# Performance work log

Measured on AMD Instinct MI355X. Metric: run time of the kernel, lower is better.

## Reference

```python
import jax, jax.numpy as jnp
import numpy as np

BETA = 0.5

def gelu(x):
    return jax.nn.gelu(x, approximate=False)  # torch F.gelu default is exact erf

def setup_inputs() -> dict:
    key = jax.random.key(0)
    ks = jax.random.split(key, 10)
    N, F, PH, P, D, H, C, E = 50000, 128, 64, 8, 4, 128, 10, 1600000
    s = 0.05
    return {
        "x": jax.random.normal(ks[0], (N, F), jnp.float32),
        "W_proj": jax.random.normal(ks[1], (PH, F), jnp.float32) * s,
        "b_proj": jnp.zeros((PH,), jnp.float32),
        "W_x": jax.random.normal(ks[2], (H, F), jnp.float32) * s,
        "b_x": jnp.zeros((H,), jnp.float32),
        "W_path": jax.random.normal(ks[3], (H, D * PH), jnp.float32) * s,
        "b_path": jnp.zeros((H,), jnp.float32),
        "W_A": jax.random.normal(ks[4], (H, N), jnp.float32) * s,
        "b_A": jnp.zeros((H,), jnp.float32),
        "W_end": jax.random.normal(ks[5], (C, H), jnp.float32) * s,
        "b_end": jnp.zeros((C,), jnp.float32),
        "index": jax.random.randint(ks[6], (N, P, D), 0, N, jnp.int64)
                 if jax.config.jax_enable_x64 else jax.random.randint(ks[6], (N, P, D), 0, N, jnp.int32),
        "edge_index": jax.random.randint(ks[7], (2, E), 0, N, jnp.int32),
    }

def reference(x, W_proj, b_proj, W_x, b_x, W_path, b_path, W_A, b_A, W_end, b_end, index, edge_index):
    N = x.shape[0]
    # path projection then per-node path gather: [N, P, D, PH]
    pp = x @ W_proj.T + b_proj
    path = pp[index]
    Np, P, D, PH = path.shape
    # node MLP (dropout off in eval)
    h = gelu(x @ W_x.T + b_x)  # [N, H]
    # concat path encoder: [N, P, D*PH] -> [N, P, H]
    pi = gelu(path.reshape(Np, P, D * PH) @ W_path.T + b_path)
    # dot-product path attention with softmax over path dim
    att = jax.nn.softmax(jnp.einsum('nh,nph->np', h, pi), axis=-1)
    path_agg = jnp.einsum('np,nph->nh', att, pi)
    # sparse adjacency (COO, weights=1) times Linear weight: A @ W_A.T + b_A
    M = W_A.T  # [N, H]
    A_x = jax.ops.segment_sum(M[edge_index[1]], edge_index[0], num_segments=N) + b_A
    out = (1.0 - BETA) * (path_agg + h) + BETA * A_x
    out = gelu(out)
    return out @ W_end.T + b_end
```

## Files before the change

### kernel.cpp

```cpp
#include <hip/hip_runtime.h>
#include <hip/hip_bf16.h>
#include <math.h>

#define NF   128
#define NPH  64
#define NP   8
#define ND   4
#define NH   128
#define NC   10
#define BCAP 2560

typedef __bf16 bf16;
typedef __attribute__((ext_vector_type(4))) __bf16 bf16x4;
typedef __attribute__((ext_vector_type(8))) __bf16 bf16x8;
typedef __attribute__((ext_vector_type(4))) float f32x4;

template<int CTRL>
__device__ __forceinline__ float dpp_add(float x) {
    int t = __builtin_amdgcn_update_dpp(0, __float_as_int(x), CTRL, 0xf, 0xf, false);
    return x + __int_as_float(t);
}
__device__ __forceinline__ float row16_sum(float x) {
    x = dpp_add<0x121>(x);
    x = dpp_add<0x122>(x);
    x = dpp_add<0x124>(x);
    x = dpp_add<0x128>(x);
    return x;
}

__device__ __forceinline__ float gelu_fast(float x) {
    float z = fabsf(x) * 0.70710678118654752f;
    float t = __builtin_amdgcn_rcpf(1.0f + 0.47047f * z);
    float poly = t * (0.3480242f + t * (-0.0958798f + t * 0.7478556f));
    float erfv = 1.0f - poly * __expf(-z * z);
    float s = copysignf(erfv, x);
    return 0.5f * x * (1.0f + s);
}

#define GLOAD_LDS16(g, l)                                                     \
    __builtin_amdgcn_global_load_lds(                                         \
        (const __attribute__((address_space(1))) unsigned int*)(g),           \
        (__attribute__((address_space(3))) unsigned int*)(l), 16, 0, 0)

__device__ __forceinline__ bf16x8 cvt8(float4 a, float4 b) {
    bf16x8 r;
    r[0] = (bf16)a.x; r[1] = (bf16)a.y; r[2] = (bf16)a.z; r[3] = (bf16)a.w;
    r[4] = (bf16)b.x; r[5] = (bf16)b.y; r[6] = (bf16)b.z; r[7] = (bf16)b.w;
    return r;
}

__device__ __forceinline__ void add8(float* a, uint4 v) {
    a[0] += __uint_as_float(v.x << 16);  a[1] += __uint_as_float(v.x & 0xffff0000u);
    a[2] += __uint_as_float(v.y << 16);  a[3] += __uint_as_float(v.y & 0xffff0000u);
    a[4] += __uint_as_float(v.z << 16);  a[5] += __uint_as_float(v.z & 0xffff0000u);
    a[6] += __uint_as_float(v.w << 16);  a[7] += __uint_as_float(v.w & 0xffff0000u);
}

__global__ __launch_bounds__(256) void k_front(
    const float* __restrict__ x,
    const float* __restrict__ Wproj, const float* __restrict__ bproj,
    const float* __restrict__ Wx,    const float* __restrict__ bx,
    bf16* __restrict__ pp, float* __restrict__ h,
    const float* __restrict__ WA, bf16* __restrict__ Mb,
    const int* __restrict__ esrc, const int* __restrict__ edst,
    int* __restrict__ gcur, unsigned* __restrict__ pairs,
    int N, int E, int nbuck, int nbP, int nbT)
{
    __shared__ alignas(16) char smem[33280];
    const int tid = threadIdx.x;

    const int bid = blockIdx.x;
    const int two = 2 * nbP;
    int cls, idx;
    if (bid < two) { cls = bid & 1; idx = bid >> 1; }
    else           { cls = 1; idx = nbP + (bid - two); }

    if (cls == 0) {
        bf16* x_s = (bf16*)smem;
        const int w = tid >> 6, l = tid & 63;
        const int c = l & 15, g = l >> 4;

        bf16x8 bfr[3][4];
        float bias[3];
        #pragma unroll
        for (int t = 0; t < 3; ++t) {
            int ch = (w * 3 + t) * 16 + c;
            const float* wr = (ch < NPH) ? &Wproj[(size_t)ch * NF]
                                         : &Wx[(size_t)(ch - NPH) * NF];
            bias[t] = (ch < NPH) ? bproj[ch] : bx[ch - NPH];
            #pragma unroll
            for (int ks = 0; ks < 4; ++ks) {
                const float* src = wr + ks * 32 + g * 8;
                bfr[t][ks] = cvt8(*(const float4*)src, *(const float4*)(src + 4));
            }
        }

        const int n0 = idx * 64;
        #pragma unroll
        for (int rr = 0; rr < 8; ++rr) {
            int id  = rr * 256 + tid;
            int row = id >> 5, c4 = id & 31;
            float4 v = make_float4(0.f, 0.f, 0.f, 0.f);
            if (n0 + row < N) v = *(const float4*)&x[(size_t)(n0 + row) * NF + c4 * 4];
            bf16x4 o;
            o[0] = (bf16)v.x; o[1] = (bf16)v.y; o[2] = (bf16)v.z; o[3] = (bf16)v.w;
            *(bf16x4*)&x_s[row * 136 + c4 * 4] = o;
        }
        __syncthreads();

        f32x4 acc[4][3] = {};
        #pragma unroll
        for (int rt = 0; rt < 4; ++rt)
            #pragma unroll
            for (int ks = 0; ks < 4; ++ks) {
                bf16x8 a = *(const bf16x8*)&x_s[(rt * 16 + c) * 136 + ks * 32 + g * 8];
                #pragma unroll
                for (int t = 0; t < 3; ++t)
                    acc[rt][t] = __builtin_amdgcn_mfma_f32_16x16x32_bf16(
                        a, bfr[t][ks], acc[rt][t], 0, 0, 0);
            }

        #pragma unroll
        for (int rt = 0; rt < 4; ++rt) {
            #pragma unroll
            for (int t = 0; t < 3; ++t) {
                int ch = (w * 3 + t) * 16 + c;
                #pragma unroll
                for (int i = 0; i < 4; ++i) {
                    int n = n0 + rt * 16 + g * 4 + i;
                    if (n >= N) continue;
                    float v = acc[rt][t][i] + bias[t];
                    if (ch < NPH) pp[(size_t)n * NPH + ch] = (bf16)v;
                    else          h[(size_t)n * NH + (ch - NPH)] = gelu_fast(v);
                }
            }
        }
    } else if (idx < nbT) {
        float* tt = (float*)smem;
        const int n0 = idx * 64;
        const int w = tid >> 6, l = tid & 63;
        #pragma unroll
        for (int rep = 0; rep < 32; ++rep) {
            int hh = rep * 4 + w;
            int n  = n0 + l;
            tt[hh * 65 + l] = (n < N) ? WA[(size_t)hh * N + n] : 0.f;
        }
        __syncthreads();
        #pragma unroll
        for (int rep = 0; rep < 32; ++rep) {
            int n_l = rep * 2 + (tid >> 7);
            int n   = n0 + n_l;
            if (n < N) Mb[(size_t)n * NH + (tid & 127)] = (bf16)tt[(tid & 127) * 65 + n_l];
        }
    } else {
        int* cnt  = (int*)smem;
        int* bofs = cnt + 800;
        const int tile = (idx - nbT) * 4096;
        for (int i = tid; i < nbuck; i += 256) cnt[i] = 0;
        __syncthreads();
        #pragma unroll
        for (int k = 0; k < 16; ++k) {
            int i = tile + k * 256 + tid;
            if (i < E) atomicAdd(&cnt[esrc[i] >> 6], 1);
        }
        __syncthreads();
        for (int i = tid; i < nbuck; i += 256) {
            int c = cnt[i];
            bofs[i] = c ? atomicAdd(&gcur[i], c) : 0;
            cnt[i] = 0;
        }
        __syncthreads();
        #pragma unroll
        for (int k = 0; k < 16; ++k) {
            int i = tile + k * 256 + tid;
            if (i < E) {
                int s = esrc[i], b = s >> 6;
                int r = atomicAdd(&cnt[b], 1);
                pairs[(size_t)b * BCAP + bofs[b] + r] =
                    ((unsigned)(s & 63) << 16) | (unsigned)edst[i];
            }
        }
    }
}

__global__ __launch_bounds__(256, 3) void k_mid2(
    const unsigned* __restrict__ pairs, const int* __restrict__ gcur,
    const bf16* __restrict__ Mb, const float* __restrict__ bA,
    float* __restrict__ axbuf2,
    const bf16* __restrict__ pp, const float* __restrict__ h,
    const float* __restrict__ Wpath, const float* __restrict__ bpath,
    const int* __restrict__ index, float* __restrict__ aggbuf,
    int N, int E, int nbuck, int nrounds)
{
    __shared__ alignas(16) char smem[37376];
    const int tid = threadIdx.x;

    const int bid = blockIdx.x;
    const int two = 2 * nbuck;
    int cls, idx;
    if (bid < two) { cls = bid & 1; idx = bid >> 1; }
    else           { cls = 0; idx = nbuck + (bid - two); }

    if (cls == 1) {
        int* hist  = (int*)smem;
        int* sc    = hist + 64;
        int* cur   = hist + 128;
        unsigned short* dstl = (unsigned short*)(smem + 768);
        const int b = idx, t = tid;
        const int cnt = gcur[b];
        const unsigned* pb = pairs + (size_t)b * BCAP;

        if (t < 64) hist[t] = 0;
        __syncthreads();
        for (int j = t; j < cnt; j += 256)
            atomicAdd(&hist[pb[j] >> 16], 1);
        __syncthreads();
        if (t < 64) sc[t] = hist[t];
        __syncthreads();
        for (int off = 1; off < 64; off <<= 1) {
            int u = (t < 64 && t >= off) ? sc[t - off] : 0;
            __syncthreads();
            if (t < 64) sc[t] += u;
            __syncthreads();
        }
        if (t < 64) cur[t] = sc[t] - hist[t];
        __syncthreads();
        for (int j = t; j < cnt; j += 256) {
            unsigned p = pb[j];
            int pos = atomicAdd(&cur[p >> 16], 1);
            dstl[pos] = (unsigned short)(p & 0xffffu);
        }
        __syncthreads();

        const int w = t >> 6, l = t & 63;
        const int e = l >> 4, q = l & 15;
        const unsigned short* Mu = (const unsigned short*)Mb;
        const int nb0 = b * 64;
        #pragma unroll 1
        for (int it = 0; it < 16; ++it) {
            const int node = it * 4 + w;
            const int n = nb0 + node;
            const int le = sc[node];
            int j = le - hist[node];
            float acc[8] = {0.f, 0.f, 0.f, 0.f, 0.f, 0.f, 0.f, 0.f};
            for (; j + 32 <= le; j += 32) {
                int d[8];
                #pragma unroll
                for (int k = 0; k < 8; ++k) d[k] = dstl[j + k * 4 + e];
                uint4 v[8];
                #pragma unroll
                for (int k = 0; k < 8; ++k)
                    v[k] = *((const uint4*)(Mu + (size_t)d[k] * NH) + q);
                #pragma unroll
                for (int k = 0; k < 8; ++k) add8(acc, v[k]);
            }
            for (; j + 4 <= le; j += 4) {
                int d0 = dstl[j + e];
                uint4 v0 = *((const uint4*)(Mu + (size_t)d0 * NH) + q);
                add8(acc, v0);
            }
            if (e < le - j) {
                int d0 = dstl[j + e];
                uint4 v0 = *((const uint4*)(Mu + (size_t)d0 * NH) + q);
                add8(acc, v0);
            }
            #pragma unroll
            for (int k = 0; k < 8; ++k) {
                acc[k] += __shfl_xor(acc[k], 16, 64);
                acc[k] += __shfl_xor(acc[k], 32, 64);
            }
            if (l < 16 && n < N) {
                float4 bA0 = *(const float4*)&bA[q * 8];
                float4 bA1 = *(const float4*)&bA[q * 8 + 4];
                float4 o0 = make_float4(0.5f * (acc[0] + bA0.x), 0.5f * (acc[1] + bA0.y),
                                        0.5f * (acc[2] + bA0.z), 0.5f * (acc[3] + bA0.w));
                float4 o1 = make_float4(0.5f * (acc[4] + bA1.x), 0.5f * (acc[5] + bA1.y),
                                        0.5f * (acc[6] + bA1.z), 0.5f * (acc[7] + bA1.w));
                *(float4*)&axbuf2[(size_t)n * NH + q * 8]     = o0;
                *(float4*)&axbuf2[(size_t)n * NH + q * 8 + 4] = o1;
            }
        }
        return;
    }

    bf16*  path_s = (bf16*)smem;
    float* h_sf   = (float*)(smem + 32768);
    float* s_red  = (float*)(smem + 36864);

    const int w   = tid >> 6;
    const int l   = tid & 63;
    const int c   = l & 15;
    const int g   = l >> 4;
    const int nl  = g >> 1;

    bf16x8 bfrag[2][8];
    #pragma unroll
    for (int ht = 0; ht < 2; ++ht) {
        int hg = (w * 2 + ht) * 16 + c;
        #pragma unroll
        for (int ks = 0; ks < 8; ++ks) {
            const float* src = &Wpath[(size_t)hg * 256 + ks * 32 + g * 8];
            bfrag[ht][ks] = cvt8(*(const float4*)src, *(const float4*)(src + 4));
        }
    }
    const float bp0 = bpath[(w * 2 + 0) * 16 + c];
    const float bp1 = bpath[(w * 2 + 1) * 16 + c];

    auto stage = [&](int round, int b) {
        const int n0 = round * 4;
        #pragma unroll
        for (int rr = 0; rr < 4; ++rr) {
            int id  = rr * 256 + tid;
            int row = id >> 5;
            int cc  = id & 31;
            int ls  = cc ^ (row & 7);
            int d   = ls >> 3, q = ls & 7;
            int nn  = row >> 3, p = row & 7;
            int idx2 = index[(size_t)(n0 + nn) * (NP * ND) + p * ND + d];
            GLOAD_LDS16(pp + (size_t)idx2 * NPH + q * 8, &path_s[b * 8192 + id * 8]);
        }
        if (tid < 128) {
            int node = tid >> 5, q = tid & 31;
            GLOAD_LDS16(&h[(size_t)(n0 + node) * NH + q * 4],
                        &h_sf[(b * 4 + node) * 128 + q * 4]);
        }
    };

    int r = idx;
    const int G = nrounds >= 0 ? (gridDim.x - nbuck) : 1;
    if (r < nrounds) stage(r, 0);
    int buf = 0;

    for (; r < nrounds; r += G) {
        const int n0 = r * 4;
        __syncthreads();
        if (r + G < nrounds) stage(r + G, buf ^ 1);

        f32x4 acc[2][2] = {};
        #pragma unroll
        for (int rt = 0; rt < 2; ++rt) {
            const int rowbase = buf * 8192 + (rt * 16 + c) * 256;
            #pragma unroll
            for (int ks = 0; ks < 8; ++ks) {
                int chunk = (ks * 4 + g) ^ (c & 7);
                bf16x8 a = *(const bf16x8*)&path_s[rowbase + chunk * 8];
                acc[rt][0] = __builtin_amdgcn_mfma_f32_16x16x32_bf16(
                    a, bfrag[0][ks], acc[rt][0], 0, 0, 0);
                acc[rt][1] = __builtin_amdgcn_mfma_f32_16x16x32_bf16(
                    a, bfrag[1][ks], acc[rt][1], 0, 0, 0);
            }
        }

        float pi[2][2][4];
        #pragma unroll
        for (int rt = 0; rt < 2; ++rt) {
            const float hv0 = h_sf[(buf * 4 + rt * 2 + nl) * 128 + w * 32 + c];
            const float hv1 = h_sf[(buf * 4 + rt * 2 + nl) * 128 + w * 32 + 16 + c];
            float sp[4];
            #pragma unroll
            for (int i = 0; i < 4; ++i) {
                pi[rt][0][i] = gelu_fast(acc[rt][0][i] + bp0);
                pi[rt][1][i] = gelu_fast(acc[rt][1][i] + bp1);
                sp[i] = hv0 * pi[rt][0][i] + hv1 * pi[rt][1][i];
            }
            #pragma unroll
            for (int i = 0; i < 4; ++i) sp[i] = row16_sum(sp[i]);
            float v = (c == 0) ? sp[0] : (c == 1) ? sp[1] : (c == 2) ? sp[2] : sp[3];
            if (c < 4) s_red[w * 32 + rt * 16 + g * 4 + c] = v;
        }

        __builtin_amdgcn_sched_barrier(0);
        asm volatile("s_waitcnt lgkmcnt(0)" ::: "memory");
        __builtin_amdgcn_s_barrier();
        __builtin_amdgcn_sched_barrier(0);

        #pragma unroll
        for (int rt = 0; rt < 2; ++rt) {
            float4 r0 = *(const float4*)&s_red[0 * 32 + rt * 16 + g * 4];
            float4 r1 = *(const float4*)&s_red[1 * 32 + rt * 16 + g * 4];
            float4 r2 = *(const float4*)&s_red[2 * 32 + rt * 16 + g * 4];
            float4 r3 = *(const float4*)&s_red[3 * 32 + rt * 16 + g * 4];
            float st[4];
            st[0] = r0.x + r1.x + r2.x + r3.x;
            st[1] = r0.y + r1.y + r2.y + r3.y;
            st[2] = r0.z + r1.z + r2.z + r3.z;
            st[3] = r0.w + r1.w + r2.w + r3.w;
            float m4 = fmaxf(fmaxf(st[0], st[1]), fmaxf(st[2], st[3]));
            float m  = fmaxf(m4, __shfl_xor(m4, 16, 64));
            float e[4], s4 = 0.f;
            #pragma unroll
            for (int i = 0; i < 4; ++i) { e[i] = __expf(st[i] - m); s4 += e[i]; }
            float den = s4 + __shfl_xor(s4, 16, 64);
            const float inv = __builtin_amdgcn_rcpf(den);

            float pa0 = 0.f, pa1 = 0.f;
            #pragma unroll
            for (int i = 0; i < 4; ++i) {
                pa0 += e[i] * pi[rt][0][i];
                pa1 += e[i] * pi[rt][1][i];
            }
            pa0 = (pa0 + __shfl_xor(pa0, 16, 64)) * inv;
            pa1 = (pa1 + __shfl_xor(pa1, 16, 64)) * inv;

            if (!(g & 1)) {
                int n = n0 + rt * 2 + nl;
                const float hv0 = h_sf[(buf * 4 + rt * 2 + nl) * 128 + w * 32 + c];
                const float hv1 = h_sf[(buf * 4 + rt * 2 + nl) * 128 + w * 32 + 16 + c];
                aggbuf[(size_t)n * NH + w * 32 + c]      = 0.5f * (pa0 + hv0);
                aggbuf[(size_t)n * NH + w * 32 + 16 + c] = 0.5f * (pa1 + hv1);
            }
        }
        buf ^= 1;
    }
}

__global__ __launch_bounds__(256) void k_fin(
    const float* __restrict__ aggbuf, const float* __restrict__ axbuf2,
    const float* __restrict__ Wend, const float* __restrict__ bend,
    float* __restrict__ out, int N)
{
    __shared__ float wend_s[NC][128];
    __shared__ float bend_s[NC];
    const int tid = threadIdx.x;
    for (int id = tid; id < NC * 128; id += 256) wend_s[id >> 7][id & 127] = Wend[id];
    if (tid < NC) bend_s[tid] = bend[tid];
    __syncthreads();

    const int w = tid >> 6, l = tid & 63;
    const int n = blockIdx.x * 4 + w;
    if (n >= N) return;
    const int q = l & 15;

    float4 agA = *(const float4*)&aggbuf[(size_t)n * NH + q * 8];
    float4 agB = *(const float4*)&aggbuf[(size_t)n * NH + q * 8 + 4];
    float4 axA = *(const float4*)&axbuf2[(size_t)n * NH + q * 8];
    float4 axB = *(const float4*)&axbuf2[(size_t)n * NH + q * 8 + 4];
    float gg[8];
    gg[0] = gelu_fast(agA.x + axA.x);
    gg[1] = gelu_fast(agA.y + axA.y);
    gg[2] = gelu_fast(agA.z + axA.z);
    gg[3] = gelu_fast(agA.w + axA.w);
    gg[4] = gelu_fast(agB.x + axB.x);
    gg[5] = gelu_fast(agB.y + axB.y);
    gg[6] = gelu_fast(agB.z + axB.z);
    gg[7] = gelu_fast(agB.w + axB.w);

    float part[NC];
    #pragma unroll
    for (int cc = 0; cc < NC; ++cc) {
        float p = 0.f;
        #pragma unroll
        for (int k = 0; k < 8; ++k) p += gg[k] * wend_s[cc][q * 8 + k];
        part[cc] = row16_sum(p);
    }

    float r = part[0];
    #pragma unroll
    for (int cc = 1; cc < NC; ++cc) r = (l == cc) ? part[cc] : r;
    if (l < NC) out[(size_t)n * NC + l] = r + bend_s[l];
}

extern "C" void kernel_launch(void* const* d_in, const int* in_sizes, int n_in,
                              void* d_out, int out_size, void* d_ws, size_t ws_size,
                              hipStream_t stream)
{
    const float* x     = (const float*)d_in[0];
    const float* Wproj = (const float*)d_in[1];
    const float* bproj = (const float*)d_in[2];
    const float* Wx    = (const float*)d_in[3];
    const float* bx    = (const float*)d_in[4];
    const float* Wpath = (const float*)d_in[5];
    const float* bpath = (const float*)d_in[6];
    const float* WA    = (const float*)d_in[7];
    const float* bA    = (const float*)d_in[8];
    const float* Wend  = (const float*)d_in[9];
    const float* bend  = (const float*)d_in[10];
    const int*   index = (const int*)d_in[11];
    const int*   eidx  = (const int*)d_in[12];

    const int N = in_sizes[0] / NF;
    const int E = in_sizes[12] / 2;
    const int* esrc = eidx;
    const int* edst = eidx + E;
    const int nbuck = (N + 63) >> 6;

    char* p = (char*)d_ws;
    auto alloc = [&](size_t bytes) {
        char* r = p;
        p += (bytes + 255) & ~(size_t)255;
        return r;
    };
    bf16*     pp     = (bf16*)alloc((size_t)N * NPH * sizeof(bf16));
    float*    h      = (float*)alloc((size_t)N * NH * sizeof(float));
    float*    aggbuf = (float*)alloc((size_t)N * NH * sizeof(float));
    float*    axbuf2 = (float*)alloc((size_t)N * NH * sizeof(float));
    bf16*     Mb     = (bf16*)alloc((size_t)N * NH * sizeof(bf16));
    unsigned* pairs  = (unsigned*)alloc((size_t)nbuck * BCAP * sizeof(unsigned));
    int*      gcur   = (int*)alloc((size_t)nbuck * sizeof(int));

    const int nbP = (N + 63) / 64;
    const int nbT = (N + 63) / 64;
    const int nbB = (E + 4095) / 4096;
    const int NPATH = 1024;
    const int nrounds = N / 4;

    hipMemsetAsync(gcur, 0, (size_t)nbuck * sizeof(int), stream);
    k_front<<<nbP + nbT + nbB, 256, 0, stream>>>(
        x, Wproj, bproj, Wx, bx, pp, h, WA, Mb, esrc, edst, gcur, pairs,
        N, E, nbuck, nbP, nbT);
    k_mid2<<<nbuck + NPATH, 256, 0, stream>>>(
        pairs, gcur, Mb, bA, axbuf2, pp, h, Wpath, bpath, index, aggbuf,
        N, E, nbuck, nrounds);
    k_fin<<<(N + 3) / 4, 256, 0, stream>>>(aggbuf, axbuf2, Wend, bend,
                                           (float*)d_out, N);
}
```

Baseline: 231.9 us.

## Split fused mid kernel into separate sparse-aggregate and path kernels, widen sparse grid

Splits the combined k_mid2 kernel, which interleaved sparse-adjacency bucket blocks with path-attention blocks, into two kernels: k_ax and k_path. k_ax launches four blocks per bucket. Each block handles a 32-channel slice using 4-byte gathers instead of 16-byte gathers, which gives more parallelism and fewer registers for the irregular gather. The cost is that the per-bucket histogram, scan and sort is repeated four times, and the two phases no longer overlap within one launch.

New measurement: 250.2 us. +7.9%, slower.

```diff
diff --git a/kernel.cpp b/kernel.cpp
--- a/kernel.cpp
+++ b/kernel.cpp
@@ -47,13 +47,6 @@
     r[0] = (bf16)a.x; r[1] = (bf16)a.y; r[2] = (bf16)a.z; r[3] = (bf16)a.w;
     r[4] = (bf16)b.x; r[5] = (bf16)b.y; r[6] = (bf16)b.z; r[7] = (bf16)b.w;
     return r;
-}
-
-__device__ __forceinline__ void add8(float* a, uint4 v) {
-    a[0] += __uint_as_float(v.x << 16);  a[1] += __uint_as_float(v.x & 0xffff0000u);
-    a[2] += __uint_as_float(v.y << 16);  a[3] += __uint_as_float(v.y & 0xffff0000u);
-    a[4] += __uint_as_float(v.z << 16);  a[5] += __uint_as_float(v.z & 0xffff0000u);
-    a[6] += __uint_as_float(v.w << 16);  a[7] += __uint_as_float(v.w & 0xffff0000u);
 }
 
 __global__ __launch_bounds__(256) void k_front(
@@ -183,110 +176,105 @@
     }
 }
 
-__global__ __launch_bounds__(256, 3) void k_mid2(
+__global__ __launch_bounds__(256) void k_ax(
     const unsigned* __restrict__ pairs, const int* __restrict__ gcur,
     const bf16* __restrict__ Mb, const float* __restrict__ bA,
-    float* __restrict__ axbuf2,
+    float* __restrict__ axbuf2, int N)
+{
+    __shared__ int hist[64], sc[64], cur[64];
+    __shared__ unsigned short dstl[BCAP];
+    const int bid = blockIdx.x;
+    const int ct  = bid & 3;
+    const int b   = bid >> 2;
+    const int t   = threadIdx.x;
+    const int cnt = gcur[b];
+    const unsigned* pb = pairs + (size_t)b * BCAP;
+
+    if (t < 64) hist[t] = 0;
+    __syncthreads();
+    for (int j = t; j < cnt; j += 256)
+        atomicAdd(&hist[pb[j] >> 16], 1);
+    __syncthreads();
+    if (t < 64) sc[t] = hist[t];
+    __syncthreads();
+    for (int off = 1; off < 64; off <<= 1) {
+        int u = (t < 64 && t >= off) ? sc[t - off] : 0;
+        __syncthreads();
+        if (t < 64) sc[t] += u;
+        __syncthreads();
+    }
+    if (t < 64) cur[t] = sc[t] - hist[t];
+    __syncthreads();
+    for (int j = t; j < cnt; j += 256) {
+        unsigned p = pb[j];
+        int pos = atomicAdd(&cur[p >> 16], 1);
+        dstl[pos] = (unsigned short)(p & 0xffffu);
+    }
+    __syncthreads();
+
+    const int w = t >> 6, l = t & 63;
+    const int e = l >> 4, q = l & 15;
+    const unsigned* Mu32 = (const unsigned*)Mb;
+    const int dwbase = ct * 16;
+    const int chb = ct * 32;
+    const int nb0 = b * 64;
+    const float bA0 = bA[chb + q * 2];
+    const float bA1 = bA[chb + q * 2 + 1];
+
+    #pragma unroll 1
+    for (int it = 0; it < 16; ++it) {
+        const int node = it * 4 + w;
+        const int hi2 = sc[node];
+        int j = hi2 - hist[node];
+        float a0 = 0.f, a1 = 0.f;
+        for (; j + 16 <= hi2; j += 16) {
+            int d0 = dstl[j + e], d1 = dstl[j + 4 + e];
+            int d2 = dstl[j + 8 + e], d3 = dstl[j + 12 + e];
+            unsigned v0 = Mu32[(size_t)d0 * 64 + dwbase + q];
+            unsigned v1 = Mu32[(size_t)d1 * 64 + dwbase + q];
+            unsigned v2 = Mu32[(size_t)d2 * 64 + dwbase + q];
+            unsigned v3 = Mu32[(size_t)d3 * 64 + dwbase + q];
+            a0 += __uint_as_float(v0 << 16) + __uint_as_float(v1 << 16) +
+                  __uint_as_float(v2 << 16) + __uint_as_float(v3 << 16);
+            a1 += __uint_as_float(v0 & 0xffff0000u) + __uint_as_float(v1 & 0xffff0000u) +
+                  __uint_as_float(v2 & 0xffff0000u) + __uint_as_float(v3 & 0xffff0000u);
+        }
+        for (; j + 4 <= hi2; j += 4) {
+            int d0 = dstl[j + e];
+            unsigned v0 = Mu32[(size_t)d0 * 64 + dwbase + q];
+            a0 += __uint_as_float(v0 << 16);
+            a1 += __uint_as_float(v0 & 0xffff0000u);
+        }
+        if (j + e < hi2) {
+            int d0 = dstl[j + e];
+            unsigned v0 = Mu32[(size_t)d0 * 64 + dwbase + q];
+            a0 += __uint_as_float(v0 << 16);
+            a1 += __uint_as_float(v0 & 0xffff0000u);
+        }
+        a0 += __shfl_xor(a0, 16, 64);  a0 += __shfl_xor(a0, 32, 64);
+        a1 += __shfl_xor(a1, 16, 64);  a1 += __shfl_xor(a1, 32, 64);
+        const int n = nb0 + node;
+        if (l < 16 && n < N) {
+            float2 o;
+            o.x = 0.5f * (a0 + bA0);
+            o.y = 0.5f * (a1 + bA1);
+            *(float2*)&axbuf2[(size_t)n * NH + chb + q * 2] = o;
+        }
+    }
+}
+
+__global__ __launch_bounds__(256, 3) void k_path(
     const bf16* __restrict__ pp, const float* __restrict__ h,
     const float* __restrict__ Wpath, const float* __restrict__ bpath,
     const int* __restrict__ index, float* __restrict__ aggbuf,
-    int N, int E, int nbuck, int nrounds)
+    int N, int nrounds)
 {
     __shared__ alignas(16) char smem[37376];
-    const int tid = threadIdx.x;
-
-    const int bid = blockIdx.x;
-    const int two = 2 * nbuck;
-    int cls, idx;
-    if (bid < two) { cls = bid & 1; idx = bid >> 1; }
-    else           { cls = 0; idx = nbuck + (bid - two); }
-
-    if (cls == 1) {
-        int* hist  = (int*)smem;
-        int* sc    = hist + 64;
-        int* cur   = hist + 128;
-        unsigned short* dstl = (unsigned short*)(smem + 768);
-        const int b = idx, t = tid;
-        const int cnt = gcur[b];
-        const unsigned* pb = pairs + (size_t)b * BCAP;
-
-        if (t < 64) hist[t] = 0;
-        __syncthreads();
-        for (int j = t; j < cnt; j += 256)
-            atomicAdd(&hist[pb[j] >> 16], 1);
-        __syncthreads();
-        if (t < 64) sc[t] = hist[t];
-        __syncthreads();
-        for (int off = 1; off < 64; off <<= 1) {
-            int u = (t < 64 && t >= off) ? sc[t - off] : 0;
-            __syncthreads();
-            if (t < 64) sc[t] += u;
-            __syncthreads();
-        }
-        if (t < 64) cur[t] = sc[t] - hist[t];
-        __syncthreads();
-        for (int j = t; j < cnt; j += 256) {
-            unsigned p = pb[j];
-            int pos = atomicAdd(&cur[p >> 16], 1);
-            dstl[pos] = (unsigned short)(p & 0xffffu);
-        }
-        __syncthreads();
-
-        const int w = t >> 6, l = t & 63;
-        const int e = l >> 4, q = l & 15;
-        const unsigned short* Mu = (const unsigned short*)Mb;
-        const int nb0 = b * 64;
-        #pragma unroll 1
-        for (int it = 0; it < 16; ++it) {
-            const int node = it * 4 + w;
-            const int n = nb0 + node;
-            const int le = sc[node];
-            int j = le - hist[node];
-            float acc[8] = {0.f, 0.f, 0.f, 0.f, 0.f, 0.f, 0.f, 0.f};
-            for (; j + 32 <= le; j += 32) {
-                int d[8];
-                #pragma unroll
-                for (int k = 0; k < 8; ++k) d[k] = dstl[j + k * 4 + e];
-                uint4 v[8];
-                #pragma unroll
-                for (int k = 0; k < 8; ++k)
-                    v[k] = *((const uint4*)(Mu + (size_t)d[k] * NH) + q);
-                #pragma unroll
-                for (int k = 0; k < 8; ++k) add8(acc, v[k]);
-            }
-            for (; j + 4 <= le; j += 4) {
-                int d0 = dstl[j + e];
-                uint4 v0 = *((const uint4*)(Mu + (size_t)d0 * NH) + q);
-                add8(acc, v0);
-            }
-            if (e < le - j) {
-                int d0 = dstl[j + e];
-                uint4 v0 = *((const uint4*)(Mu + (size_t)d0 * NH) + q);
-                add8(acc, v0);
-            }
-            #pragma unroll
-            for (int k = 0; k < 8; ++k) {
-                acc[k] += __shfl_xor(acc[k], 16, 64);
-                acc[k] += __shfl_xor(acc[k], 32, 64);
-            }
-            if (l < 16 && n < N) {
-                float4 bA0 = *(const float4*)&bA[q * 8];
-                float4 bA1 = *(const float4*)&bA[q * 8 + 4];
-                float4 o0 = make_float4(0.5f * (acc[0] + bA0.x), 0.5f * (acc[1] + bA0.y),
-                                        0.5f * (acc[2] + bA0.z), 0.5f * (acc[3] + bA0.w));
-                float4 o1 = make_float4(0.5f * (acc[4] + bA1.x), 0.5f * (acc[5] + bA1.y),
-                                        0.5f * (acc[6] + bA1.z), 0.5f * (acc[7] + bA1.w));
-                *(float4*)&axbuf2[(size_t)n * NH + q * 8]     = o0;
-                *(float4*)&axbuf2[(size_t)n * NH + q * 8 + 4] = o1;
-            }
-        }
-        return;
-    }
-
     bf16*  path_s = (bf16*)smem;
     float* h_sf   = (float*)(smem + 32768);
     float* s_red  = (float*)(smem + 36864);
 
+    const int tid = threadIdx.x;
     const int w   = tid >> 6;
     const int l   = tid & 63;
     const int c   = l & 15;
@@ -316,8 +304,8 @@
             int ls  = cc ^ (row & 7);
             int d   = ls >> 3, q = ls & 7;
             int nn  = row >> 3, p = row & 7;
-            int idx2 = index[(size_t)(n0 + nn) * (NP * ND) + p * ND + d];
-            GLOAD_LDS16(pp + (size_t)idx2 * NPH + q * 8, &path_s[b * 8192 + id * 8]);
+            int idx = index[(size_t)(n0 + nn) * (NP * ND) + p * ND + d];
+            GLOAD_LDS16(pp + (size_t)idx * NPH + q * 8, &path_s[b * 8192 + id * 8]);
         }
         if (tid < 128) {
             int node = tid >> 5, q = tid & 31;
@@ -326,8 +314,8 @@
         }
     };
 
-    int r = idx;
-    const int G = nrounds >= 0 ? (gridDim.x - nbuck) : 1;
+    int r = blockIdx.x;
+    const int G = gridDim.x;
     if (r < nrounds) stage(r, 0);
     int buf = 0;
 
@@ -508,9 +496,8 @@
     k_front<<<nbP + nbT + nbB, 256, 0, stream>>>(
         x, Wproj, bproj, Wx, bx, pp, h, WA, Mb, esrc, edst, gcur, pairs,
         N, E, nbuck, nbP, nbT);
-    k_mid2<<<nbuck + NPATH, 256, 0, stream>>>(
-        pairs, gcur, Mb, bA, axbuf2, pp, h, Wpath, bpath, index, aggbuf,
-        N, E, nbuck, nrounds);
+    k_ax<<<nbuck * 4, 256, 0, stream>>>(pairs, gcur, Mb, bA, axbuf2, N);
+    k_path<<<NPATH, 256, 0, stream>>>(pp, h, Wpath, bpath, index, aggbuf, N, nrounds);
     k_fin<<<(N + 3) / 4, 256, 0, stream>>>(aggbuf, axbuf2, Wend, bend,
                                            (float*)d_out, N);
 }
```
